# Kernel optimization log

Measured on AMD Instinct MI355X. Metric: run time of the kernel, lower is better.

## Reference

```python
import jax, jax.numpy as jnp
import numpy as np

N = 100000
E = 1600000
IN_CH = 128
HEADS = 4
OUT_CH = 32


def setup_inputs() -> dict:
    key = jax.random.key(0)
    k1, k2, k3, k4, k5, k6 = jax.random.split(key, 6)
    x = jax.random.normal(k1, (N, IN_CH), dtype=jnp.float32)
    edge_attr = jax.random.normal(k2, (E,), dtype=jnp.float32)
    edge_index = jax.random.randint(k3, (2, E), 0, N, dtype=jnp.int64)
    # xavier-uniform-ish parameter init
    def xavier(k, shape):
        fan_in, fan_out = shape[-1], shape[-2] if len(shape) > 1 else shape[-1]
        lim = jnp.sqrt(6.0 / (fan_in + fan_out)).astype(jnp.float32)
        return jax.random.uniform(k, shape, jnp.float32, -lim, lim)
    lin_w = xavier(k4, (HEADS * OUT_CH, IN_CH))       # nn.Linear weight [out,in]
    lin_edge_w = xavier(k5, (HEADS * OUT_CH, 1))      # [out,1]
    att = xavier(k6, (1, HEADS, 3 * OUT_CH))
    return {"x": x, "edge_attr": edge_attr, "edge_index": edge_index,
            "lin_w": lin_w, "lin_edge_w": lin_edge_w, "att": att}


def reference(x, edge_attr, edge_index, lin_w, lin_edge_w, att):
    n = x.shape[0]
    # node transform: [N, H, C]
    xh = (x @ lin_w.T).reshape(n, HEADS, OUT_CH)
    # edge transform: [E, H, C]
    eh = (edge_attr[:, None] @ lin_edge_w.T).reshape(-1, HEADS, OUT_CH)
    row, col = edge_index[0], edge_index[1]
    # split att into source/dest/edge parts to avoid materializing cat([x_i,x_j,e])
    att_i, att_j, att_e = jnp.split(att, 3, axis=-1)  # each [1, H, C]
    # per-edge attention logits: [E, H]
    alpha = ((xh[row] * att_i).sum(-1)
             + (xh[col] * att_j).sum(-1)
             + (eh * att_e).sum(-1))
    alpha = jax.nn.leaky_relu(alpha, negative_slope=0.2)
    # segment softmax over destination node (row)
    amax = jax.ops.segment_max(alpha, row, num_segments=n)           # [N, H]
    amax = jnp.where(jnp.isfinite(amax), amax, 0.0)
    ex = jnp.exp(alpha - amax[row])
    den = jax.ops.segment_sum(ex, row, num_segments=n)               # [N, H]
    alpha = ex / (den[row] + 1e-16)
    # weighted message scatter-add: [N, H, C]
    out = jax.ops.segment_sum(alpha[..., None] * xh[col], row, num_segments=n)
    # concat heads
    return out.reshape(n, HEADS * OUT_CH)
```

## Files before the change

kernel.cpp:

```cpp
#include <hip/hip_runtime.h>

#define HEADS 4
#define OUT_CH 32
#define HC 128
#define INC 128
#define CAP 48

__device__ __forceinline__ unsigned short f2bf(float f) {
  unsigned int u = __float_as_uint(f);
  unsigned int r = (u + 0x7FFFu + ((u >> 16) & 1u)) >> 16;
  return (unsigned short)r;
}

__global__ void ce_kernel(const float* __restrict__ lew,
                          const float* __restrict__ att,
                          float* __restrict__ ce) {
  int h = threadIdx.x;
  if (h < HEADS) {
    float s = 0.f;
    for (int c = 0; c < OUT_CH; ++c)
      s += lew[h * OUT_CH + c] * att[h * 96 + 2 * OUT_CH + c];
    ce[h] = s;
  }
}

#define TM 64
__global__ __launch_bounds__(256) void gemm_build(
    const float* __restrict__ x, const float* __restrict__ W,
    const float* __restrict__ att, const int* __restrict__ ei,
    const float* __restrict__ ea, unsigned short* __restrict__ xhb,
    float* __restrict__ si, float* __restrict__ sj, int* __restrict__ cnt,
    unsigned int* __restrict__ slots, int nrows, int E, int G) {
  __shared__ float As[TM][68];
  __shared__ float Bs[128][68];

  if (blockIdx.x >= G) {
    int e = (blockIdx.x - G) * 256 + threadIdx.x;
    if (e < E) {
      int r = ei[e];
      int c = ei[E + e];
      unsigned int u = __float_as_uint(ea[e]);
      unsigned int word = ((u + 0x10000u) & 0xFFFE0000u) | (unsigned int)c;
      int pos = atomicAdd(&cnt[r], 1);
      if (pos < CAP) slots[(size_t)r * CAP + pos] = word;
    }
    return;
  }

  const int tid = threadIdx.x;
  const int row0 = blockIdx.x * TM;
  const int og = tid & 15;
  const int ng = tid >> 4;

  float acc[4][8];
#pragma unroll
  for (int i = 0; i < 4; i++)
#pragma unroll
    for (int j = 0; j < 8; j++) acc[i][j] = 0.f;

  for (int ks = 0; ks < 128; ks += 64) {
    __syncthreads();
#pragma unroll
    for (int t = 0; t < 4; t++) {
      int i4 = tid + t * 256;
      int r = i4 >> 4;
      int k4 = i4 & 15;
      int gr = row0 + r;
      float4 v = make_float4(0.f, 0.f, 0.f, 0.f);
      if (gr < nrows) v = ((const float4*)x)[(size_t)gr * 32 + (ks >> 2) + k4];
      *(float4*)&As[r][k4 * 4] = v;
    }
#pragma unroll
    for (int t = 0; t < 8; t++) {
      int i4 = tid + t * 256;
      int o = i4 >> 4;
      int k4 = i4 & 15;
      float4 v = ((const float4*)W)[(size_t)o * 32 + (ks >> 2) + k4];
      *(float4*)&Bs[o][k4 * 4] = v;
    }
    __syncthreads();

    for (int k = 0; k < 64; k += 4) {
      float4 a[4], b[8];
#pragma unroll
      for (int i = 0; i < 4; i++) a[i] = *(const float4*)&As[ng * 4 + i][k];
#pragma unroll
      for (int j = 0; j < 8; j++) b[j] = *(const float4*)&Bs[og + 16 * j][k];
#pragma unroll
      for (int i = 0; i < 4; i++)
#pragma unroll
        for (int j = 0; j < 8; j++) {
          acc[i][j] += a[i].x * b[j].x;
          acc[i][j] += a[i].y * b[j].y;
          acc[i][j] += a[i].z * b[j].z;
          acc[i][j] += a[i].w * b[j].w;
        }
    }
  }

  float ai[8], aj[8];
#pragma unroll
  for (int j = 0; j < 8; j++) {
    int ch = og + 16 * j;
    int h = ch >> 5, c = ch & 31;
    ai[j] = att[h * 96 + c];
    aj[j] = att[h * 96 + 32 + c];
  }
#pragma unroll
  for (int i = 0; i < 4; i++) {
    float ph_i[4] = {0.f, 0.f, 0.f, 0.f};
    float ph_j[4] = {0.f, 0.f, 0.f, 0.f};
#pragma unroll
    for (int j = 0; j < 8; j++) {
      int h = (og + 16 * j) >> 5;
      ph_i[h] += acc[i][j] * ai[j];
      ph_j[h] += acc[i][j] * aj[j];
    }
#pragma unroll
    for (int h = 0; h < 4; h++) {
#pragma unroll
      for (int off = 8; off >= 1; off >>= 1) {
        ph_i[h] += __shfl_down(ph_i[h], off, 16);
        ph_j[h] += __shfl_down(ph_j[h], off, 16);
      }
    }
    int gr = row0 + ng * 4 + i;
    if (og == 0 && gr < nrows) {
#pragma unroll
      for (int h = 0; h < 4; h++) {
        si[(size_t)gr * 4 + h] = ph_i[h];
        sj[(size_t)gr * 4 + h] = ph_j[h];
      }
    }
  }

  __syncthreads();
  unsigned short* xs = (unsigned short*)As;
#pragma unroll
  for (int i = 0; i < 4; i++)
#pragma unroll
    for (int j = 0; j < 8; j++)
      xs[(ng * 4 + i) * 128 + og + 16 * j] = f2bf(acc[i][j]);
  __syncthreads();
  const uint4* src = (const uint4*)xs;
#pragma unroll
  for (int t = 0; t < 4; t++) {
    int idx = tid + t * 256;
    int r = idx >> 4, q = idx & 15;
    int gr = row0 + r;
    if (gr < nrows) ((uint4*)(xhb + (size_t)gr * 128))[q] = src[idx];
  }
}

__global__ __launch_bounds__(256) void gather_kernel(
    const int* __restrict__ cnt, const unsigned int* __restrict__ slots,
    const float* __restrict__ si, const float* __restrict__ sj,
    const float* __restrict__ ce, const unsigned short* __restrict__ xhb,
    float* __restrict__ out, int n) {
  int node = blockIdx.x * 4 + (threadIdx.x >> 6);
  if (node >= n) return;
  int lane = threadIdx.x & 63;
  int h = lane >> 4;
  float si_h = si[(size_t)node * 4 + h];
  float ce_h = ce[h];
  int m = cnt[node];
  if (m > CAP) m = CAP;
  const unsigned int* sl = slots + (size_t)node * CAP;

  float acc0 = 0.f, acc1 = 0.f, wsum = 0.f;
  int i = 0;
  for (; i + 4 <= m; i += 4) {
    uint4 ww = *(const uint4*)(sl + i);
    int c0 = ww.x & 0x1FFFF, c1 = ww.y & 0x1FFFF;
    int c2 = ww.z & 0x1FFFF, c3 = ww.w & 0x1FFFF;
    float t0 = si_h + sj[(size_t)c0 * 4 + h] +
               __uint_as_float(ww.x & 0xFFFE0000u) * ce_h;
    float t1 = si_h + sj[(size_t)c1 * 4 + h] +
               __uint_as_float(ww.y & 0xFFFE0000u) * ce_h;
    float t2 = si_h + sj[(size_t)c2 * 4 + h] +
               __uint_as_float(ww.z & 0xFFFE0000u) * ce_h;
    float t3 = si_h + sj[(size_t)c3 * 4 + h] +
               __uint_as_float(ww.w & 0xFFFE0000u) * ce_h;
    t0 = t0 > 0.f ? t0 : 0.2f * t0;
    t1 = t1 > 0.f ? t1 : 0.2f * t1;
    t2 = t2 > 0.f ? t2 : 0.2f * t2;
    t3 = t3 > 0.f ? t3 : 0.2f * t3;
    float w0 = __expf(t0), w1 = __expf(t1), w2 = __expf(t2), w3 = __expf(t3);
    unsigned int x0 = *(const unsigned int*)(xhb + (size_t)c0 * 128 + lane * 2);
    unsigned int x1 = *(const unsigned int*)(xhb + (size_t)c1 * 128 + lane * 2);
    unsigned int x2 = *(const unsigned int*)(xhb + (size_t)c2 * 128 + lane * 2);
    unsigned int x3 = *(const unsigned int*)(xhb + (size_t)c3 * 128 + lane * 2);
    acc0 += w0 * __uint_as_float(x0 << 16) + w1 * __uint_as_float(x1 << 16) +
            w2 * __uint_as_float(x2 << 16) + w3 * __uint_as_float(x3 << 16);
    acc1 += w0 * __uint_as_float(x0 & 0xFFFF0000u) +
            w1 * __uint_as_float(x1 & 0xFFFF0000u) +
            w2 * __uint_as_float(x2 & 0xFFFF0000u) +
            w3 * __uint_as_float(x3 & 0xFFFF0000u);
    wsum += w0 + w1 + w2 + w3;
  }
  for (; i < m; ++i) {
    unsigned int w = sl[i];
    int c0 = w & 0x1FFFF;
    float t0 = si_h + sj[(size_t)c0 * 4 + h] +
               __uint_as_float(w & 0xFFFE0000u) * ce_h;
    t0 = t0 > 0.f ? t0 : 0.2f * t0;
    float w0 = __expf(t0);
    unsigned int x0 = *(const unsigned int*)(xhb + (size_t)c0 * 128 + lane * 2);
    acc0 += w0 * __uint_as_float(x0 << 16);
    acc1 += w0 * __uint_as_float(x0 & 0xFFFF0000u);
    wsum += w0;
  }
  float inv = 1.0f / (wsum + 1e-16f);
  float2 o;
  o.x = acc0 * inv;
  o.y = acc1 * inv;
  *(float2*)(out + (size_t)node * HC + lane * 2) = o;
}

extern "C" void kernel_launch(void* const* d_in, const int* in_sizes, int n_in,
                              void* d_out, int out_size, void* d_ws,
                              size_t ws_size, hipStream_t stream) {
  const float* x = (const float*)d_in[0];
  const float* edge_attr = (const float*)d_in[1];
  const int* ei = (const int*)d_in[2];
  const float* lin_w = (const float*)d_in[3];
  const float* lew = (const float*)d_in[4];
  const float* att = (const float*)d_in[5];
  float* out = (float*)d_out;

  const int N = in_sizes[0] / INC;
  const int E = in_sizes[1];

  unsigned int* slots = (unsigned int*)d_ws;
  unsigned short* xhb = (unsigned short*)(slots + (size_t)N * CAP);
  float* si = (float*)(xhb + (size_t)N * 128);
  float* sj = si + (size_t)N * 4;
  float* ce = sj + (size_t)N * 4;
  int* cnt = (int*)(ce + 16);

  hipMemsetAsync(cnt, 0, (size_t)N * sizeof(int), stream);
  ce_kernel<<<1, 64, 0, stream>>>(lew, att, ce);

  const int G = (N + TM - 1) / TM;
  const int B = (E + 255) / 256;
  gemm_build<<<G + B, 256, 0, stream>>>(x, lin_w, att, ei, edge_attr, xhb, si,
                                        sj, cnt, slots, N, E, G);
  gather_kernel<<<(N + 3) / 4, 256, 0, stream>>>(cnt, slots, si, sj, ce, xhb,
                                                 out, N);
}
```

Measured before the change: 312.3 us.

## Use bf16 MFMA for node GEMM and dedupe per-edge logit computation in gather

Replaces the fp32 shared-memory SIMT GEMM with per-wave bf16 MFMA 16x16x32 tiles. A prep kernel pre-converts W to bf16, and x is converted to bf16 while staged in LDS, which cuts LDS traffic and ALU work. In the gather kernel each lane now computes one of the 16 (edge, head) logits per 4-edge chunk and broadcasts the weights with shuffles, instead of every lane redoing exp and sj loads for four edges. The GEMM inputs are now quantised to bf16, which changes precision, and W is loaded straight from global memory without LDS reuse.

```diff
diff --git a/kernel.cpp b/kernel.cpp
--- a/kernel.cpp
+++ b/kernel.cpp
@@ -6,33 +6,44 @@
 #define INC 128
 #define CAP 48
 
+typedef __attribute__((ext_vector_type(8))) short bfrag;
+typedef __attribute__((ext_vector_type(4))) float ffrag;
+
+union U16 { uint4 u; bfrag f; };
+
 __device__ __forceinline__ unsigned short f2bf(float f) {
   unsigned int u = __float_as_uint(f);
   unsigned int r = (u + 0x7FFFu + ((u >> 16) & 1u)) >> 16;
   return (unsigned short)r;
 }
 
-__global__ void ce_kernel(const float* __restrict__ lew,
-                          const float* __restrict__ att,
-                          float* __restrict__ ce) {
-  int h = threadIdx.x;
-  if (h < HEADS) {
+__global__ void prep_kernel(const float* __restrict__ W,
+                            const float* __restrict__ lew,
+                            const float* __restrict__ att,
+                            unsigned short* __restrict__ Wb,
+                            float* __restrict__ ce) {
+  int tid = threadIdx.x;
+#pragma unroll
+  for (int t = 0; t < 64; t++) {
+    int idx = tid + t * 256;
+    Wb[idx] = f2bf(W[idx]);
+  }
+  if (tid < HEADS) {
     float s = 0.f;
     for (int c = 0; c < OUT_CH; ++c)
-      s += lew[h * OUT_CH + c] * att[h * 96 + 2 * OUT_CH + c];
-    ce[h] = s;
-  }
-}
-
-#define TM 64
+      s += lew[tid * OUT_CH + c] * att[tid * 96 + 2 * OUT_CH + c];
+    ce[tid] = s;
+  }
+}
+
+#define APITCH 136
 __global__ __launch_bounds__(256) void gemm_build(
-    const float* __restrict__ x, const float* __restrict__ W,
+    const float* __restrict__ x, const unsigned short* __restrict__ Wb,
     const float* __restrict__ att, const int* __restrict__ ei,
     const float* __restrict__ ea, unsigned short* __restrict__ xhb,
     float* __restrict__ si, float* __restrict__ sj, int* __restrict__ cnt,
     unsigned int* __restrict__ slots, int nrows, int E, int G) {
-  __shared__ float As[TM][68];
-  __shared__ float Bs[128][68];
+  __shared__ unsigned short Als[4][16 * APITCH];
 
   if (blockIdx.x >= G) {
     int e = (blockIdx.x - G) * 256 + threadIdx.x;
@@ -48,84 +59,70 @@
   }
 
   const int tid = threadIdx.x;
-  const int row0 = blockIdx.x * TM;
-  const int og = tid & 15;
-  const int ng = tid >> 4;
-
-  float acc[4][8];
-#pragma unroll
-  for (int i = 0; i < 4; i++)
-#pragma unroll
-    for (int j = 0; j < 8; j++) acc[i][j] = 0.f;
-
-  for (int ks = 0; ks < 128; ks += 64) {
-    __syncthreads();
-#pragma unroll
-    for (int t = 0; t < 4; t++) {
-      int i4 = tid + t * 256;
-      int r = i4 >> 4;
-      int k4 = i4 & 15;
-      int gr = row0 + r;
-      float4 v = make_float4(0.f, 0.f, 0.f, 0.f);
-      if (gr < nrows) v = ((const float4*)x)[(size_t)gr * 32 + (ks >> 2) + k4];
-      *(float4*)&As[r][k4 * 4] = v;
-    }
-#pragma unroll
-    for (int t = 0; t < 8; t++) {
-      int i4 = tid + t * 256;
-      int o = i4 >> 4;
-      int k4 = i4 & 15;
-      float4 v = ((const float4*)W)[(size_t)o * 32 + (ks >> 2) + k4];
-      *(float4*)&Bs[o][k4 * 4] = v;
-    }
-    __syncthreads();
-
-    for (int k = 0; k < 64; k += 4) {
-      float4 a[4], b[8];
-#pragma unroll
-      for (int i = 0; i < 4; i++) a[i] = *(const float4*)&As[ng * 4 + i][k];
-#pragma unroll
-      for (int j = 0; j < 8; j++) b[j] = *(const float4*)&Bs[og + 16 * j][k];
-#pragma unroll
-      for (int i = 0; i < 4; i++)
-#pragma unroll
-        for (int j = 0; j < 8; j++) {
-          acc[i][j] += a[i].x * b[j].x;
-          acc[i][j] += a[i].y * b[j].y;
-          acc[i][j] += a[i].z * b[j].z;
-          acc[i][j] += a[i].w * b[j].w;
-        }
+  const int wid = tid >> 6;
+  const int lane = tid & 63;
+  const int row0 = blockIdx.x * 64 + wid * 16;
+  if (row0 >= nrows) return;
+  unsigned short* As = &Als[wid][0];
+
+#pragma unroll
+  for (int t = 0; t < 8; t++) {
+    int idx = t * 64 + lane;
+    int r = idx >> 5;
+    int q = idx & 31;
+    int gr = row0 + r;
+    float4 v = make_float4(0.f, 0.f, 0.f, 0.f);
+    if (gr < nrows) v = ((const float4*)x)[(size_t)gr * 32 + q];
+    unsigned int p0 = ((unsigned int)f2bf(v.y) << 16) | f2bf(v.x);
+    unsigned int p1 = ((unsigned int)f2bf(v.w) << 16) | f2bf(v.z);
+    *(uint2*)&As[r * APITCH + q * 4] = make_uint2(p0, p1);
+  }
+
+  const int m15 = lane & 15;
+  const int g = lane >> 4;
+
+  ffrag acc[8];
+#pragma unroll
+  for (int t = 0; t < 8; t++) acc[t] = (ffrag){0.f, 0.f, 0.f, 0.f};
+
+#pragma unroll
+  for (int ks = 0; ks < 4; ks++) {
+    U16 a;
+    a.u = *(const uint4*)&As[m15 * APITCH + ks * 32 + g * 8];
+#pragma unroll
+    for (int nt = 0; nt < 8; nt++) {
+      U16 b;
+      b.u = *(const uint4*)&Wb[(size_t)(nt * 16 + m15) * 128 + ks * 32 + g * 8];
+      acc[nt] = __builtin_amdgcn_mfma_f32_16x16x32_bf16(a.f, b.f, acc[nt],
+                                                        0, 0, 0);
     }
   }
 
   float ai[8], aj[8];
 #pragma unroll
-  for (int j = 0; j < 8; j++) {
-    int ch = og + 16 * j;
-    int h = ch >> 5, c = ch & 31;
-    ai[j] = att[h * 96 + c];
-    aj[j] = att[h * 96 + 32 + c];
-  }
-#pragma unroll
-  for (int i = 0; i < 4; i++) {
-    float ph_i[4] = {0.f, 0.f, 0.f, 0.f};
-    float ph_j[4] = {0.f, 0.f, 0.f, 0.f};
-#pragma unroll
-    for (int j = 0; j < 8; j++) {
-      int h = (og + 16 * j) >> 5;
-      ph_i[h] += acc[i][j] * ai[j];
-      ph_j[h] += acc[i][j] * aj[j];
-    }
+  for (int t = 0; t < 8; t++) {
+    int h = t >> 1, c = (t & 1) * 16 + m15;
+    ai[t] = att[h * 96 + c];
+    aj[t] = att[h * 96 + 32 + c];
+  }
+#pragma unroll
+  for (int reg = 0; reg < 4; reg++) {
+    float ph_i[4], ph_j[4];
 #pragma unroll
     for (int h = 0; h < 4; h++) {
-#pragma unroll
-      for (int off = 8; off >= 1; off >>= 1) {
+      ph_i[h] = acc[2 * h][reg] * ai[2 * h] + acc[2 * h + 1][reg] * ai[2 * h + 1];
+      ph_j[h] = acc[2 * h][reg] * aj[2 * h] + acc[2 * h + 1][reg] * aj[2 * h + 1];
+    }
+#pragma unroll
+    for (int off = 8; off >= 1; off >>= 1) {
+#pragma unroll
+      for (int h = 0; h < 4; h++) {
         ph_i[h] += __shfl_down(ph_i[h], off, 16);
         ph_j[h] += __shfl_down(ph_j[h], off, 16);
       }
     }
-    int gr = row0 + ng * 4 + i;
-    if (og == 0 && gr < nrows) {
+    int gr = row0 + g * 4 + reg;
+    if (m15 == 0 && gr < nrows) {
 #pragma unroll
       for (int h = 0; h < 4; h++) {
         si[(size_t)gr * 4 + h] = ph_i[h];
@@ -134,18 +131,19 @@
     }
   }
 
-  __syncthreads();
-  unsigned short* xs = (unsigned short*)As;
-#pragma unroll
-  for (int i = 0; i < 4; i++)
-#pragma unroll
-    for (int j = 0; j < 8; j++)
-      xs[(ng * 4 + i) * 128 + og + 16 * j] = f2bf(acc[i][j]);
-  __syncthreads();
-  const uint4* src = (const uint4*)xs;
+#pragma unroll
+  for (int t = 0; t < 8; t++) {
+#pragma unroll
+    for (int reg = 0; reg < 4; reg++) {
+      int r = g * 4 + reg;
+      int n = t * 16 + m15;
+      As[r * 128 + n] = f2bf(acc[t][reg]);
+    }
+  }
+  const uint4* src = (const uint4*)As;
 #pragma unroll
   for (int t = 0; t < 4; t++) {
-    int idx = tid + t * 256;
+    int idx = t * 64 + lane;
     int r = idx >> 4, q = idx & 15;
     int gr = row0 + r;
     if (gr < nrows) ((uint4*)(xhb + (size_t)gr * 128))[q] = src[idx];
@@ -161,31 +159,35 @@
   if (node >= n) return;
   int lane = threadIdx.x & 63;
   int h = lane >> 4;
-  float si_h = si[(size_t)node * 4 + h];
-  float ce_h = ce[h];
+  float4 si4 = *(const float4*)(si + (size_t)node * 4);
+  float4 ce4 = *(const float4*)ce;
   int m = cnt[node];
   if (m > CAP) m = CAP;
   const unsigned int* sl = slots + (size_t)node * CAP;
+
+  int q = lane & 15;
+  int kq = q >> 2;
+  int hq = q & 3;
+  float si_q = hq == 0 ? si4.x : (hq == 1 ? si4.y : (hq == 2 ? si4.z : si4.w));
+  float ce_q = hq == 0 ? ce4.x : (hq == 1 ? ce4.y : (hq == 2 ? ce4.z : ce4.w));
 
   float acc0 = 0.f, acc1 = 0.f, wsum = 0.f;
   int i = 0;
   for (; i + 4 <= m; i += 4) {
     uint4 ww = *(const uint4*)(sl + i);
+    unsigned int wsel =
+        kq == 0 ? ww.x : (kq == 1 ? ww.y : (kq == 2 ? ww.z : ww.w));
+    int cq = wsel & 0x1FFFF;
+    float t = si_q + sj[(size_t)cq * 4 + hq] +
+              __uint_as_float(wsel & 0xFFFE0000u) * ce_q;
+    t = t > 0.f ? t : 0.2f * t;
+    float wq = __expf(t);
+    float w0 = __shfl(wq, h);
+    float w1 = __shfl(wq, 4 + h);
+    float w2 = __shfl(wq, 8 + h);
+    float w3 = __shfl(wq, 12 + h);
     int c0 = ww.x & 0x1FFFF, c1 = ww.y & 0x1FFFF;
     int c2 = ww.z & 0x1FFFF, c3 = ww.w & 0x1FFFF;
-    float t0 = si_h + sj[(size_t)c0 * 4 + h] +
-               __uint_as_float(ww.x & 0xFFFE0000u) * ce_h;
-    float t1 = si_h + sj[(size_t)c1 * 4 + h] +
-               __uint_as_float(ww.y & 0xFFFE0000u) * ce_h;
-    float t2 = si_h + sj[(size_t)c2 * 4 + h] +
-               __uint_as_float(ww.z & 0xFFFE0000u) * ce_h;
-    float t3 = si_h + sj[(size_t)c3 * 4 + h] +
-               __uint_as_float(ww.w & 0xFFFE0000u) * ce_h;
-    t0 = t0 > 0.f ? t0 : 0.2f * t0;
-    t1 = t1 > 0.f ? t1 : 0.2f * t1;
-    t2 = t2 > 0.f ? t2 : 0.2f * t2;
-    t3 = t3 > 0.f ? t3 : 0.2f * t3;
-    float w0 = __expf(t0), w1 = __expf(t1), w2 = __expf(t2), w3 = __expf(t3);
     unsigned int x0 = *(const unsigned int*)(xhb + (size_t)c0 * 128 + lane * 2);
     unsigned int x1 = *(const unsigned int*)(xhb + (size_t)c1 * 128 + lane * 2);
     unsigned int x2 = *(const unsigned int*)(xhb + (size_t)c2 * 128 + lane * 2);
@@ -198,6 +200,8 @@
             w3 * __uint_as_float(x3 & 0xFFFF0000u);
     wsum += w0 + w1 + w2 + w3;
   }
+  float si_h = h == 0 ? si4.x : (h == 1 ? si4.y : (h == 2 ? si4.z : si4.w));
+  float ce_h = h == 0 ? ce4.x : (h == 1 ? ce4.y : (h == 2 ? ce4.z : ce4.w));
   for (; i < m; ++i) {
     unsigned int w = sl[i];
     int c0 = w & 0x1FFFF;
@@ -236,14 +240,15 @@
   float* si = (float*)(xhb + (size_t)N * 128);
   float* sj = si + (size_t)N * 4;
   float* ce = sj + (size_t)N * 4;
-  int* cnt = (int*)(ce + 16);
+  unsigned short* Wb = (unsigned short*)(ce + 16);
+  int* cnt = (int*)(Wb + 16384);
 
   hipMemsetAsync(cnt, 0, (size_t)N * sizeof(int), stream);
-  ce_kernel<<<1, 64, 0, stream>>>(lew, att, ce);
-
-  const int G = (N + TM - 1) / TM;
+  prep_kernel<<<1, 256, 0, stream>>>(lin_w, lew, att, Wb, ce);
+
+  const int G = (N + 63) / 64;
   const int B = (E + 255) / 256;
-  gemm_build<<<G + B, 256, 0, stream>>>(x, lin_w, att, ei, edge_attr, xhb, si,
+  gemm_build<<<G + B, 256, 0, stream>>>(x, Wb, att, ei, edge_attr, xhb, si,
                                         sj, cnt, slots, N, E, G);
   gather_kernel<<<(N + 3) / 4, 256, 0, stream>>>(cnt, slots, si, sj, ce, xhb,
                                                  out, N);
```

Result: faster. 296.2 us (-5.2%).
